# Optimization experiments

Hardware: AMD Instinct MI355X
Metric: run time of the kernel (lower is better)

## Reference

```python
import jax, jax.numpy as jnp
import numpy as np

BOX = 256          # box_size
N_CLASSES = 2      # n_classes
BATCH = 2
N_PTS = 262144


def setup_inputs() -> dict:
    key = jax.random.key(0)
    k1, k2 = jax.random.split(key)
    # points are normalized coordinates in [-0.5, 0.5)
    points = jax.random.uniform(k1, (BATCH, N_PTS, 3), dtype=jnp.float32,
                                minval=-0.5, maxval=0.499)
    values = jax.random.normal(k2, (BATCH, N_CLASSES, N_PTS), dtype=jnp.float32)
    return {"points": points, "values": values}


def reference(points, values):
    """Trilinear (CIC) scatter of per-point, per-class values into a 3D volume.

    points: [B, N, 3] in [-0.5, 0.5);  values: [B, C, N]
    returns vol: [B, C, box, box, box]
    """
    box = BOX
    V = box ** 3
    B, N, _ = points.shape
    C = values.shape[1]

    p = (points + 0.5) * box                 # [B, N, 3] voxel-space coords
    base = jnp.floor(p)
    r = p - base                              # fractional part, [B, N, 3]
    base = base.astype(jnp.int32)

    idx_list, w_list = [], []
    for dx in (0, 1):
        for dy in (0, 1):
            for dz in (0, 1):
                off_i = jnp.array([dx, dy, dz], dtype=jnp.int32)
                off_f = jnp.array([dx, dy, dz], dtype=r.dtype)
                c = base + off_i                                   # [B, N, 3]
                # per-axis weight: (1-d) + (2d-1)*r  == (1-r) if d=0 else r
                w = jnp.prod(1.0 - off_f + (2.0 * off_f - 1.0) * r, axis=-1)  # [B, N]
                x_, y_, z_ = c[..., 0], c[..., 1], c[..., 2]
                valid = ((x_ >= 0) & (x_ < box) & (y_ >= 0) & (y_ < box)
                         & (z_ >= 0) & (z_ < box))
                # out-of-range corners are redirected to index 0 with weight 0
                idx = ((z_ * box + y_) * box + x_) * valid.astype(jnp.int32)
                idx_list.append(idx)
                w_list.append(w * valid.astype(w.dtype))

    idx8 = jnp.concatenate(idx_list, axis=1)   # [B, 8N]
    w8 = jnp.concatenate(w_list, axis=1)       # [B, 8N]
    vals8 = jnp.tile(values, (1, 1, 8))        # [B, C, 8N]
    src = w8[:, None, :] * vals8               # [B, C, 8N]

    def scatter_one(idx_b, src_b):
        # idx_b: [8N], src_b: [C, 8N] -> [C, V]
        return jnp.zeros((C, V), src_b.dtype).at[:, idx_b].add(src_b)

    vol = jax.vmap(scatter_one)(idx8, src)     # [B, C, V]
    return vol.reshape(B, C, box, box, box)
```

## Files before the change

### kernel.cpp

```cpp
#include <hip/hip_runtime.h>

#define BOX   256
#define NCLS  2
#define BATCH 2
#define NPTS  262144
#define VOL   (BOX * BOX * BOX)
#define NBINS (BATCH * BOX * BOX)
#define CAP   32
#define CAPSH 5
#define RY    16
#define NT    (BOX / RY)
#define NREG  (BATCH * BOX * NT)
#define NBMETA 34

__global__ __launch_bounds__(256) void k_place(const float* __restrict__ pts,
                                               const float* __restrict__ vals,
                                               unsigned* __restrict__ cursor,
                                               float4* __restrict__ rec,
                                               float4* __restrict__ ovf4,
                                               unsigned* __restrict__ ovfbin,
                                               unsigned* __restrict__ ovfcnt)
{
    const int tid = blockIdx.x * 256 + threadIdx.x;
    const int b = tid >> 18;
    const int n = tid & (NPTS - 1);

    const float* pp = pts + ((size_t)b * NPTS + n) * 3;
    const float px = (pp[0] + 0.5f) * (float)BOX;
    const float py = (pp[1] + 0.5f) * (float)BOX;
    const float pz = (pp[2] + 0.5f) * (float)BOX;

    const float fy = floorf(py), fz = floorf(pz);
    const int by = (int)fy, bz = (int)fz;
    const float ry = py - fy, rz = pz - fz;

    const unsigned qy = (unsigned)(ry * 65536.0f);
    const unsigned qz = (unsigned)(rz * 65536.0f);
    const unsigned packed = (qz << 16) | (qy & 0xffffu);

    const float v0 = vals[((size_t)b * NCLS + 0) * NPTS + n];
    const float v1 = vals[((size_t)b * NCLS + 1) * NPTS + n];
    const float4 r = make_float4(px, __uint_as_float(packed), v0, v1);

    const unsigned bin = ((unsigned)b << 16) | ((unsigned)bz << 8) | (unsigned)by;
    const unsigned slot = atomicAdd(&cursor[bin], 1u);
    if (slot < CAP) {
        rec[((size_t)bin << CAPSH) + slot] = r;
    } else {
        const unsigned o = atomicAdd(ovfcnt, 1u);
        ovf4[o] = r;
        ovfbin[o] = bin;
    }
}

__global__ __launch_bounds__(512) void k_region(const float4* __restrict__ rec,
                                                const unsigned* __restrict__ cursor,
                                                const float4* __restrict__ ovf4,
                                                const unsigned* __restrict__ ovfbin,
                                                const unsigned* __restrict__ ovfcnt,
                                                float* __restrict__ out)
{
    __shared__ float acc[NCLS * RY * BOX];
    __shared__ unsigned s_bin[NBMETA];
    __shared__ unsigned s_len[NBMETA];
    __shared__ unsigned s_pfx[NBMETA + 1];

    const int tid = threadIdx.x;
    const int bid = blockIdx.x;
    const int b = bid >> 12;
    const int P = (bid >> 4) & 255;
    const int T = bid & 15;

    {
        float4* a4 = (float4*)acc;
        #pragma unroll
        for (int i = 0; i < 4; ++i)
            a4[i * 512 + tid] = make_float4(0.f, 0.f, 0.f, 0.f);
    }

    if (tid < NBMETA) {
        const int j = tid;
        const int zsrc = P - 1 + (j >= 17 ? 1 : 0);
        const int y0 = RY * T - 1 + (j >= 17 ? j - 17 : j);
        unsigned bin = 0, len = 0;
        if (zsrc >= 0 && y0 >= 0 && y0 < BOX) {
            bin = ((unsigned)b << 16) | ((unsigned)zsrc << 8) | (unsigned)y0;
            len = cursor[bin];
            if (len > CAP) len = CAP;
        }
        s_bin[j] = bin;
        s_len[j] = len;
    }
    __syncthreads();

    if (tid < 64) {
        const unsigned own = (tid < NBMETA) ? s_len[tid] : 0u;
        unsigned v = own;
        #pragma unroll
        for (int off = 1; off < 64; off <<= 1) {
            const unsigned t = __shfl_up(v, off, 64);
            if (tid >= off) v += t;
        }
        if (tid < NBMETA) s_pfx[tid] = v - own;
        if (tid == NBMETA - 1) s_pfx[NBMETA] = v;
    }
    __syncthreads();

    const int R = (int)s_pfx[NBMETA];
    for (int r = tid; r < R; r += 512) {
        int lo = 0, hi = NBMETA - 1;
        while (lo < hi) {
            const int mid = (lo + hi + 1) >> 1;
            if ((int)s_pfx[mid] <= r) lo = mid; else hi = mid - 1;
        }
        const size_t idx = ((size_t)s_bin[lo] << CAPSH) + (unsigned)(r - (int)s_pfx[lo]);
        const float4 q = rec[idx];

        const unsigned pk = __float_as_uint(q.y);
        const float ry = (float)(pk & 0xffffu) * (1.0f / 65536.0f);
        const float rz = (float)(pk >> 16) * (1.0f / 65536.0f);
        const float fx = floorf(q.x);
        const float rx = q.x - fx;
        const int ix = (int)fx;

        const float wz = (lo >= 17) ? (1.0f - rz) : rz;
        const int yy0 = (lo >= 17 ? lo - 17 : lo) - 1;

        #pragma unroll
        for (int dy = 0; dy < 2; ++dy) {
            const int yy = yy0 + dy;
            if ((unsigned)yy < RY) {
                const float wzy = wz * (dy ? ry : 1.0f - ry);
                #pragma unroll
                for (int dx = 0; dx < 2; ++dx) {
                    const int x = ix + dx;
                    if (x < BOX) {
                        const float w = wzy * (dx ? rx : 1.0f - rx);
                        const int li = yy * BOX + x;
                        atomicAdd(&acc[li], w * q.z);
                        atomicAdd(&acc[RY * BOX + li], w * q.w);
                    }
                }
            }
        }
    }

    const int oc = (int)*ovfcnt;
    for (int r = tid; r < oc; r += 512) {
        const unsigned bin = ovfbin[r];
        if ((int)(bin >> 16) != b) continue;
        const int bz = (int)((bin >> 8) & 255u);
        if (bz != P && bz != P - 1) continue;
        const int by = (int)(bin & 255u);
        const int yy0 = by - RY * T;
        if (yy0 < -1 || yy0 > RY - 1) continue;

        const float4 q = ovf4[r];
        const unsigned pk = __float_as_uint(q.y);
        const float ry = (float)(pk & 0xffffu) * (1.0f / 65536.0f);
        const float rz = (float)(pk >> 16) * (1.0f / 65536.0f);
        const float fx = floorf(q.x);
        const float rx = q.x - fx;
        const int ix = (int)fx;
        const float wz = (bz == P) ? (1.0f - rz) : rz;

        for (int dy = 0; dy < 2; ++dy) {
            const int yy = yy0 + dy;
            if ((unsigned)yy < RY) {
                const float wzy = wz * (dy ? ry : 1.0f - ry);
                for (int dx = 0; dx < 2; ++dx) {
                    const int x = ix + dx;
                    if (x < BOX) {
                        const float w = wzy * (dx ? rx : 1.0f - rx);
                        const int li = yy * BOX + x;
                        atomicAdd(&acc[li], w * q.z);
                        atomicAdd(&acc[RY * BOX + li], w * q.w);
                    }
                }
            }
        }
    }
    __syncthreads();

    #pragma unroll
    for (int c = 0; c < NCLS; ++c) {
        const size_t o4base = (size_t)((b * NCLS + c) * BOX + P) * (BOX * BOX / 4)
                              + (size_t)T * (RY * BOX / 4);
        float4* o4 = (float4*)out;
        const float4* a4 = (const float4*)(acc + c * RY * BOX);
        #pragma unroll
        for (int i = 0; i < 2; ++i)
            o4[o4base + i * 512 + tid] = a4[i * 512 + tid];
    }
}

__global__ __launch_bounds__(256) void cic_scatter_kernel(
    const float* __restrict__ points, const float* __restrict__ values,
    float* __restrict__ out)
{
    const int tid = blockIdx.x * blockDim.x + threadIdx.x;
    if (tid >= BATCH * NPTS) return;
    const int b = tid >> 18, n = tid & (NPTS - 1);
    const float* pp = points + ((size_t)b * NPTS + n) * 3;
    const float px = (pp[0] + 0.5f) * BOX, py = (pp[1] + 0.5f) * BOX, pz = (pp[2] + 0.5f) * BOX;
    const float fx = floorf(px), fy = floorf(py), fz = floorf(pz);
    const float rx = px - fx, ry = py - fy, rz = pz - fz;
    const int ix = (int)fx, iy = (int)fy, iz = (int)fz;
    const float v0 = values[((size_t)b * NCLS + 0) * NPTS + n];
    const float v1 = values[((size_t)b * NCLS + 1) * NPTS + n];
    const float wx[2] = {1.f - rx, rx}, wy[2] = {1.f - ry, ry}, wz[2] = {1.f - rz, rz};
    float* out0 = out + ((size_t)b * NCLS + 0) * (size_t)VOL;
    float* out1 = out + ((size_t)b * NCLS + 1) * (size_t)VOL;
    for (int dz = 0; dz < 2; ++dz) {
        const int z = iz + dz; if (z >= BOX) continue;
        for (int dy = 0; dy < 2; ++dy) {
            const int y = iy + dy; if (y >= BOX) continue;
            const float wzy = wz[dz] * wy[dy];
            const int rowbase = (z * BOX + y) * BOX;
            for (int dx = 0; dx < 2; ++dx) {
                const int x = ix + dx; if (x >= BOX) continue;
                atomicAdd(out0 + rowbase + x, wzy * wx[dx] * v0);
                atomicAdd(out1 + rowbase + x, wzy * wx[dx] * v1);
            }
        }
    }
}

extern "C" void kernel_launch(void* const* d_in, const int* in_sizes, int n_in,
                              void* d_out, int out_size, void* d_ws, size_t ws_size,
                              hipStream_t stream) {
    const float* points = (const float*)d_in[0];
    const float* values = (const float*)d_in[1];
    float* out = (float*)d_out;

    const size_t CUR_OFF  = 0;
    const size_t OVFC_OFF = (size_t)NBINS * 4;
    const size_t REC_OFF  = OVFC_OFF + 256;
    const size_t OVF4_OFF = REC_OFF + (size_t)NBINS * CAP * 16;
    const size_t OVFB_OFF = OVF4_OFF + (size_t)BATCH * NPTS * 16;
    const size_t WS_NEED  = OVFB_OFF + (size_t)BATCH * NPTS * 4;

    if (ws_size < WS_NEED) {
        hipMemsetAsync(out, 0, (size_t)out_size * sizeof(float), stream);
        cic_scatter_kernel<<<(BATCH * NPTS) / 256, 256, 0, stream>>>(points, values, out);
        return;
    }

    char* ws = (char*)d_ws;
    unsigned* cursor = (unsigned*)(ws + CUR_OFF);
    unsigned* ovfcnt = (unsigned*)(ws + OVFC_OFF);
    float4*   rec    = (float4*)(ws + REC_OFF);
    float4*   ovf4   = (float4*)(ws + OVF4_OFF);
    unsigned* ovfbin = (unsigned*)(ws + OVFB_OFF);

    hipMemsetAsync(ws, 0, OVFC_OFF + 256, stream);

    k_place<<<(BATCH * NPTS) / 256, 256, 0, stream>>>(points, values, cursor,
                                                      rec, ovf4, ovfbin, ovfcnt);
    k_region<<<NREG, 512, 0, stream>>>(rec, cursor, ovf4, ovfbin, ovfcnt, out);
}
```

Baseline: 112.8 us.

## Replace per-bin atomic binning with two-level block-local counting sort

Points are binned with a two-pass counting sort instead of one global atomic per point into fixed 32-slot bins. The first pass does a block-local histogram over coarse (batch, z-pair) groups, then coalesced staged writes. The second pass sorts each group by fine (z parity, y) bin and emits bin start and count tables. The region kernel then reads two contiguous ranges with no prefix-sum or binary search. Records now pack integer x plus quantized fractions. The cost is an extra kernel and another full pass over the records, and x precision drops to 15 bits.

```diff
diff --git a/kernel.cpp b/kernel.cpp
--- a/kernel.cpp
+++ b/kernel.cpp
@@ -1,71 +1,190 @@
 #include <hip/hip_runtime.h>
 
-#define BOX   256
-#define NCLS  2
-#define BATCH 2
-#define NPTS  262144
-#define VOL   (BOX * BOX * BOX)
-#define NBINS (BATCH * BOX * BOX)
-#define CAP   32
-#define CAPSH 5
-#define RY    16
-#define NT    (BOX / RY)
-#define NREG  (BATCH * BOX * NT)
-#define NBMETA 34
-
-__global__ __launch_bounds__(256) void k_place(const float* __restrict__ pts,
-                                               const float* __restrict__ vals,
-                                               unsigned* __restrict__ cursor,
-                                               float4* __restrict__ rec,
-                                               float4* __restrict__ ovf4,
-                                               unsigned* __restrict__ ovfbin,
-                                               unsigned* __restrict__ ovfcnt)
-{
-    const int tid = blockIdx.x * 256 + threadIdx.x;
-    const int b = tid >> 18;
-    const int n = tid & (NPTS - 1);
-
-    const float* pp = pts + ((size_t)b * NPTS + n) * 3;
-    const float px = (pp[0] + 0.5f) * (float)BOX;
-    const float py = (pp[1] + 0.5f) * (float)BOX;
-    const float pz = (pp[2] + 0.5f) * (float)BOX;
-
-    const float fy = floorf(py), fz = floorf(pz);
-    const int by = (int)fy, bz = (int)fz;
-    const float ry = py - fy, rz = pz - fz;
-
-    const unsigned qy = (unsigned)(ry * 65536.0f);
-    const unsigned qz = (unsigned)(rz * 65536.0f);
-    const unsigned packed = (qz << 16) | (qy & 0xffffu);
-
-    const float v0 = vals[((size_t)b * NCLS + 0) * NPTS + n];
-    const float v1 = vals[((size_t)b * NCLS + 1) * NPTS + n];
-    const float4 r = make_float4(px, __uint_as_float(packed), v0, v1);
-
-    const unsigned bin = ((unsigned)b << 16) | ((unsigned)bz << 8) | (unsigned)by;
-    const unsigned slot = atomicAdd(&cursor[bin], 1u);
-    if (slot < CAP) {
-        rec[((size_t)bin << CAPSH) + slot] = r;
-    } else {
-        const unsigned o = atomicAdd(ovfcnt, 1u);
-        ovf4[o] = r;
-        ovfbin[o] = bin;
-    }
-}
-
-__global__ __launch_bounds__(512) void k_region(const float4* __restrict__ rec,
-                                                const unsigned* __restrict__ cursor,
-                                                const float4* __restrict__ ovf4,
+#define BOX    256
+#define NCLS   2
+#define BATCH  2
+#define NPTS   262144
+#define VOL    (BOX * BOX * BOX)
+#define NPTOT  (BATCH * NPTS)
+#define NGRP   256
+#define GCAP   3584
+#define NFINE  512
+#define NBINS  (NGRP * NFINE)
+#define L1PTS  2048
+#define L1BLK  (NPTOT / L1PTS)
+#define RY     16
+#define NREG   (BATCH * BOX * (BOX / RY))
+
+__global__ __launch_bounds__(512) void k_zero(unsigned* __restrict__ p)
+{
+    p[threadIdx.x] = 0u;
+}
+
+__global__ __launch_bounds__(256) void k_l1(const float* __restrict__ pts,
+                                            const float* __restrict__ vals,
+                                            unsigned* __restrict__ gcur,
+                                            uint4* __restrict__ rec1,
+                                            uint4* __restrict__ ovf4,
+                                            unsigned* __restrict__ ovfbin,
+                                            unsigned* __restrict__ ovfcnt)
+{
+    __shared__ unsigned hist[256];
+    __shared__ unsigned excl[256];
+    __shared__ unsigned cur[256];
+    __shared__ unsigned gbase[256];
+    __shared__ uint4 stag[L1PTS];
+
+    const int t = threadIdx.x;
+    hist[t] = 0;
+    __syncthreads();
+
+    uint4 rec[8];
+    unsigned bkt[8];
+    const int base = blockIdx.x * L1PTS;
+    #pragma unroll
+    for (int k = 0; k < 8; ++k) {
+        const int gp = base + k * 256 + t;
+        const int b = gp >> 18;
+        const int n = gp & (NPTS - 1);
+        const float* pp = pts + (size_t)gp * 3;
+        const float px = (pp[0] + 0.5f) * 256.0f;
+        const float py = (pp[1] + 0.5f) * 256.0f;
+        const float pz = (pp[2] + 0.5f) * 256.0f;
+        const float fx = floorf(px), fy = floorf(py), fz = floorf(pz);
+        const int ix = (int)fx, by = (int)fy, bz = (int)fz;
+        const unsigned qx = (unsigned)((px - fx) * 32768.0f);
+        const unsigned qy = (unsigned)((py - fy) * 65536.0f);
+        const unsigned qz = (unsigned)((pz - fz) * 65536.0f);
+        const float v0 = vals[(size_t)(b * 2) * NPTS + n];
+        const float v1 = vals[(size_t)(b * 2 + 1) * NPTS + n];
+        rec[k].x = (unsigned)ix | (qx << 8) | ((unsigned)(bz & 1) << 23)
+                 | ((unsigned)by << 24);
+        rec[k].y = (qy & 0xffffu) | (qz << 16);
+        rec[k].z = __float_as_uint(v0);
+        rec[k].w = __float_as_uint(v1);
+        bkt[k] = ((unsigned)b << 7) | ((unsigned)bz >> 1);
+        atomicAdd(&hist[bkt[k]], 1u);
+    }
+    __syncthreads();
+
+    const unsigned own = hist[t];
+    for (int off = 1; off < 256; off <<= 1) {
+        unsigned v = 0;
+        if (t >= off) v = hist[t - off];
+        __syncthreads();
+        hist[t] += v;
+        __syncthreads();
+    }
+    const unsigned incl = hist[t];
+    const unsigned ex = incl - own;
+    excl[t] = ex;
+    cur[t] = ex;
+    if (own) gbase[t] = atomicAdd(&gcur[t], own);
+    __syncthreads();
+
+    #pragma unroll
+    for (int k = 0; k < 8; ++k) {
+        const unsigned s = atomicAdd(&cur[bkt[k]], 1u);
+        stag[s] = rec[k];
+    }
+    __syncthreads();
+
+    for (int s = t; s < L1PTS; s += 256) {
+        int lo = 0, hi = 255;
+        while (lo < hi) {
+            const int mid = (lo + hi) >> 1;
+            if (cur[mid] > (unsigned)s) hi = mid; else lo = mid + 1;
+        }
+        const unsigned rel = s - excl[lo];
+        const unsigned gaddr = gbase[lo] + rel;
+        const uint4 r = stag[s];
+        if (gaddr < GCAP) {
+            rec1[(size_t)lo * GCAP + gaddr] = r;
+        } else {
+            const unsigned o = atomicAdd(ovfcnt, 1u);
+            const unsigned zl = (r.x >> 23) & 1u;
+            const unsigned by = r.x >> 24;
+            ovf4[o] = r;
+            ovfbin[o] = ((unsigned)lo << 9) | (zl << 8) | by;
+        }
+    }
+}
+
+__global__ __launch_bounds__(512) void k_l2(const uint4* __restrict__ rec1,
+                                            const unsigned* __restrict__ gcur,
+                                            uint4* __restrict__ rec2,
+                                            unsigned* __restrict__ binStart,
+                                            unsigned* __restrict__ binCnt)
+{
+    __shared__ unsigned hist[NFINE];
+    __shared__ unsigned excl[NFINE];
+    __shared__ unsigned cur[NFINE];
+    __shared__ uint4 stag[GCAP];
+
+    const int t = threadIdx.x;
+    const int g = blockIdx.x;
+    hist[t] = 0;
+    __syncthreads();
+
+    unsigned cnt = gcur[g];
+    if (cnt > GCAP) cnt = GCAP;
+
+    uint4 rec[7];
+    unsigned fk[7];
+    #pragma unroll
+    for (int k = 0; k < 7; ++k) {
+        const int s = t + k * 512;
+        if (s < (int)cnt) {
+            const uint4 r = rec1[(size_t)g * GCAP + s];
+            const unsigned key = (((r.x >> 23) & 1u) << 8) | (r.x >> 24);
+            rec[k] = r; fk[k] = key;
+            atomicAdd(&hist[key], 1u);
+        }
+    }
+    __syncthreads();
+
+    const unsigned own = hist[t];
+    for (int off = 1; off < 512; off <<= 1) {
+        unsigned v = 0;
+        if (t >= off) v = hist[t - off];
+        __syncthreads();
+        hist[t] += v;
+        __syncthreads();
+    }
+    const unsigned incl = hist[t];
+    const unsigned ex = incl - own;
+    excl[t] = ex;
+    cur[t] = ex;
+    binStart[(g << 9) + t] = (unsigned)(g * GCAP) + ex;
+    binCnt[(g << 9) + t] = own;
+    __syncthreads();
+
+    #pragma unroll
+    for (int k = 0; k < 7; ++k) {
+        const int s = t + k * 512;
+        if (s < (int)cnt) {
+            const unsigned sl = atomicAdd(&cur[fk[k]], 1u);
+            stag[sl] = rec[k];
+        }
+    }
+    __syncthreads();
+
+    for (int s = t; s < (int)cnt; s += 512)
+        rec2[(size_t)g * GCAP + s] = stag[s];
+}
+
+__global__ __launch_bounds__(512) void k_region(const uint4* __restrict__ rec2,
+                                                const unsigned* __restrict__ binStart,
+                                                const unsigned* __restrict__ binCnt,
+                                                const uint4* __restrict__ ovf4,
                                                 const unsigned* __restrict__ ovfbin,
                                                 const unsigned* __restrict__ ovfcnt,
                                                 float* __restrict__ out)
 {
     __shared__ float acc[NCLS * RY * BOX];
-    __shared__ unsigned s_bin[NBMETA];
-    __shared__ unsigned s_len[NBMETA];
-    __shared__ unsigned s_pfx[NBMETA + 1];
-
-    const int tid = threadIdx.x;
+    __shared__ unsigned meta[4];
+
+    const int t = threadIdx.x;
     const int bid = blockIdx.x;
     const int b = bid >> 12;
     const int P = (bid >> 4) & 255;
@@ -75,56 +194,39 @@
         float4* a4 = (float4*)acc;
         #pragma unroll
         for (int i = 0; i < 4; ++i)
-            a4[i * 512 + tid] = make_float4(0.f, 0.f, 0.f, 0.f);
-    }
-
-    if (tid < NBMETA) {
-        const int j = tid;
-        const int zsrc = P - 1 + (j >= 17 ? 1 : 0);
-        const int y0 = RY * T - 1 + (j >= 17 ? j - 17 : j);
-        unsigned bin = 0, len = 0;
-        if (zsrc >= 0 && y0 >= 0 && y0 < BOX) {
-            bin = ((unsigned)b << 16) | ((unsigned)zsrc << 8) | (unsigned)y0;
-            len = cursor[bin];
-            if (len > CAP) len = CAP;
-        }
-        s_bin[j] = bin;
-        s_len[j] = len;
-    }
-    __syncthreads();
-
-    if (tid < 64) {
-        const unsigned own = (tid < NBMETA) ? s_len[tid] : 0u;
-        unsigned v = own;
-        #pragma unroll
-        for (int off = 1; off < 64; off <<= 1) {
-            const unsigned t = __shfl_up(v, off, 64);
-            if (tid >= off) v += t;
-        }
-        if (tid < NBMETA) s_pfx[tid] = v - own;
-        if (tid == NBMETA - 1) s_pfx[NBMETA] = v;
-    }
-    __syncthreads();
-
-    const int R = (int)s_pfx[NBMETA];
-    for (int r = tid; r < R; r += 512) {
-        int lo = 0, hi = NBMETA - 1;
-        while (lo < hi) {
-            const int mid = (lo + hi + 1) >> 1;
-            if ((int)s_pfx[mid] <= r) lo = mid; else hi = mid - 1;
-        }
-        const size_t idx = ((size_t)s_bin[lo] << CAPSH) + (unsigned)(r - (int)s_pfx[lo]);
-        const float4 q = rec[idx];
-
-        const unsigned pk = __float_as_uint(q.y);
-        const float ry = (float)(pk & 0xffffu) * (1.0f / 65536.0f);
-        const float rz = (float)(pk >> 16) * (1.0f / 65536.0f);
-        const float fx = floorf(q.x);
-        const float rx = q.x - fx;
-        const int ix = (int)fx;
-
-        const float wz = (lo >= 17) ? (1.0f - rz) : rz;
-        const int yy0 = (lo >= 17 ? lo - 17 : lo) - 1;
+            a4[i * 512 + t] = make_float4(0.f, 0.f, 0.f, 0.f);
+    }
+    if (t < 2) {
+        const int zsrc = P - 1 + t;
+        unsigned s = 0, e = 0;
+        if (zsrc >= 0) {
+            int ylo = 16 * T - 1; if (ylo < 0) ylo = 0;
+            const int yhi = 16 * T + 15;
+            const unsigned fb_lo = ((unsigned)b << 16) | ((unsigned)zsrc << 8) | (unsigned)ylo;
+            const unsigned fb_hi = ((unsigned)b << 16) | ((unsigned)zsrc << 8) | (unsigned)yhi;
+            s = binStart[fb_lo];
+            e = binStart[fb_hi] + binCnt[fb_hi];
+        }
+        meta[2 * t] = s; meta[2 * t + 1] = e;
+    }
+    __syncthreads();
+
+    const unsigned s1 = meta[0], e1 = meta[1], s2 = meta[2], e2 = meta[3];
+    const int n1 = (int)(e1 - s1), n2 = (int)(e2 - s2), n = n1 + n2;
+
+    for (int r = t; r < n; r += 512) {
+        const int inP = (r >= n1);
+        const unsigned idx = inP ? (s2 + (unsigned)(r - n1)) : (s1 + (unsigned)r);
+        const uint4 q = rec2[idx];
+        const int ix = (int)(q.x & 255u);
+        const float rx = (float)((q.x >> 8) & 0x7fffu) * (1.0f / 32768.0f);
+        const int by = (int)(q.x >> 24);
+        const float ry = (float)(q.y & 0xffffu) * (1.0f / 65536.0f);
+        const float rz = (float)(q.y >> 16) * (1.0f / 65536.0f);
+        const float v0 = __uint_as_float(q.z);
+        const float v1 = __uint_as_float(q.w);
+        const float wz = inP ? (1.0f - rz) : rz;
+        const int yy0 = by - 16 * T;
 
         #pragma unroll
         for (int dy = 0; dy < 2; ++dy) {
@@ -137,8 +239,8 @@
                     if (x < BOX) {
                         const float w = wzy * (dx ? rx : 1.0f - rx);
                         const int li = yy * BOX + x;
-                        atomicAdd(&acc[li], w * q.z);
-                        atomicAdd(&acc[RY * BOX + li], w * q.w);
+                        atomicAdd(&acc[li], w * v0);
+                        atomicAdd(&acc[RY * BOX + li], w * v1);
                     }
                 }
             }
@@ -146,24 +248,20 @@
     }
 
     const int oc = (int)*ovfcnt;
-    for (int r = tid; r < oc; r += 512) {
-        const unsigned bin = ovfbin[r];
-        if ((int)(bin >> 16) != b) continue;
-        const int bz = (int)((bin >> 8) & 255u);
+    for (int r = t; r < oc; r += 512) {
+        const unsigned fb = ovfbin[r];
+        if ((int)(fb >> 16) != b) continue;
+        const int bz = (int)((fb >> 8) & 255u);
         if (bz != P && bz != P - 1) continue;
-        const int by = (int)(bin & 255u);
-        const int yy0 = by - RY * T;
+        const int by = (int)(fb & 255u);
+        const int yy0 = by - 16 * T;
         if (yy0 < -1 || yy0 > RY - 1) continue;
-
-        const float4 q = ovf4[r];
-        const unsigned pk = __float_as_uint(q.y);
-        const float ry = (float)(pk & 0xffffu) * (1.0f / 65536.0f);
-        const float rz = (float)(pk >> 16) * (1.0f / 65536.0f);
-        const float fx = floorf(q.x);
-        const float rx = q.x - fx;
-        const int ix = (int)fx;
+        const uint4 q = ovf4[r];
+        const int ix = (int)(q.x & 255u);
+        const float rx = (float)((q.x >> 8) & 0x7fffu) * (1.0f / 32768.0f);
+        const float ry = (float)(q.y & 0xffffu) * (1.0f / 65536.0f);
+        const float rz = (float)(q.y >> 16) * (1.0f / 65536.0f);
         const float wz = (bz == P) ? (1.0f - rz) : rz;
-
         for (int dy = 0; dy < 2; ++dy) {
             const int yy = yy0 + dy;
             if ((unsigned)yy < RY) {
@@ -173,8 +271,8 @@
                     if (x < BOX) {
                         const float w = wzy * (dx ? rx : 1.0f - rx);
                         const int li = yy * BOX + x;
-                        atomicAdd(&acc[li], w * q.z);
-                        atomicAdd(&acc[RY * BOX + li], w * q.w);
+                        atomicAdd(&acc[li], w * __uint_as_float(q.z));
+                        atomicAdd(&acc[RY * BOX + li], w * __uint_as_float(q.w));
                     }
                 }
             }
@@ -190,7 +288,7 @@
         const float4* a4 = (const float4*)(acc + c * RY * BOX);
         #pragma unroll
         for (int i = 0; i < 2; ++i)
-            o4[o4base + i * 512 + tid] = a4[i * 512 + tid];
+            o4[o4base + i * 512 + t] = a4[i * 512 + t];
     }
 }
 
@@ -199,18 +297,18 @@
     float* __restrict__ out)
 {
     const int tid = blockIdx.x * blockDim.x + threadIdx.x;
-    if (tid >= BATCH * NPTS) return;
+    if (tid >= NPTOT) return;
     const int b = tid >> 18, n = tid & (NPTS - 1);
-    const float* pp = points + ((size_t)b * NPTS + n) * 3;
+    const float* pp = points + (size_t)tid * 3;
     const float px = (pp[0] + 0.5f) * BOX, py = (pp[1] + 0.5f) * BOX, pz = (pp[2] + 0.5f) * BOX;
     const float fx = floorf(px), fy = floorf(py), fz = floorf(pz);
     const float rx = px - fx, ry = py - fy, rz = pz - fz;
     const int ix = (int)fx, iy = (int)fy, iz = (int)fz;
-    const float v0 = values[((size_t)b * NCLS + 0) * NPTS + n];
-    const float v1 = values[((size_t)b * NCLS + 1) * NPTS + n];
+    const float v0 = values[(size_t)(b * 2) * NPTS + n];
+    const float v1 = values[(size_t)(b * 2 + 1) * NPTS + n];
     const float wx[2] = {1.f - rx, rx}, wy[2] = {1.f - ry, ry}, wz[2] = {1.f - rz, rz};
-    float* out0 = out + ((size_t)b * NCLS + 0) * (size_t)VOL;
-    float* out1 = out + ((size_t)b * NCLS + 1) * (size_t)VOL;
+    float* out0 = out + (size_t)(b * 2) * VOL;
+    float* out1 = out + (size_t)(b * 2 + 1) * VOL;
     for (int dz = 0; dz < 2; ++dz) {
         const int z = iz + dz; if (z >= BOX) continue;
         for (int dy = 0; dy < 2; ++dy) {
@@ -233,29 +331,34 @@
     const float* values = (const float*)d_in[1];
     float* out = (float*)d_out;
 
-    const size_t CUR_OFF  = 0;
-    const size_t OVFC_OFF = (size_t)NBINS * 4;
-    const size_t REC_OFF  = OVFC_OFF + 256;
-    const size_t OVF4_OFF = REC_OFF + (size_t)NBINS * CAP * 16;
-    const size_t OVFB_OFF = OVF4_OFF + (size_t)BATCH * NPTS * 16;
-    const size_t WS_NEED  = OVFB_OFF + (size_t)BATCH * NPTS * 4;
+    const size_t GCUR_OFF = 0;
+    const size_t OVFC_OFF = 1024;
+    const size_t REC1_OFF = 4096;
+    const size_t REC2_OFF = REC1_OFF + (size_t)NGRP * GCAP * 16;
+    const size_t BST_OFF  = REC2_OFF + (size_t)NGRP * GCAP * 16;
+    const size_t BCT_OFF  = BST_OFF + (size_t)NBINS * 4;
+    const size_t OVF4_OFF = BCT_OFF + (size_t)NBINS * 4;
+    const size_t OVFB_OFF = OVF4_OFF + (size_t)NPTOT * 16;
+    const size_t WS_NEED  = OVFB_OFF + (size_t)NPTOT * 4;
 
     if (ws_size < WS_NEED) {
         hipMemsetAsync(out, 0, (size_t)out_size * sizeof(float), stream);
-        cic_scatter_kernel<<<(BATCH * NPTS) / 256, 256, 0, stream>>>(points, values, out);
+        cic_scatter_kernel<<<NPTOT / 256, 256, 0, stream>>>(points, values, out);
         return;
     }
 
     char* ws = (char*)d_ws;
-    unsigned* cursor = (unsigned*)(ws + CUR_OFF);
-    unsigned* ovfcnt = (unsigned*)(ws + OVFC_OFF);
-    float4*   rec    = (float4*)(ws + REC_OFF);
-    float4*   ovf4   = (float4*)(ws + OVF4_OFF);
-    unsigned* ovfbin = (unsigned*)(ws + OVFB_OFF);
-
-    hipMemsetAsync(ws, 0, OVFC_OFF + 256, stream);
-
-    k_place<<<(BATCH * NPTS) / 256, 256, 0, stream>>>(points, values, cursor,
-                                                      rec, ovf4, ovfbin, ovfcnt);
-    k_region<<<NREG, 512, 0, stream>>>(rec, cursor, ovf4, ovfbin, ovfcnt, out);
-}
+    unsigned* gcur     = (unsigned*)(ws + GCUR_OFF);
+    unsigned* ovfcnt   = (unsigned*)(ws + OVFC_OFF);
+    uint4*    rec1     = (uint4*)(ws + REC1_OFF);
+    uint4*    rec2     = (uint4*)(ws + REC2_OFF);
+    unsigned* binStart = (unsigned*)(ws + BST_OFF);
+    unsigned* binCnt   = (unsigned*)(ws + BCT_OFF);
+    uint4*    ovf4     = (uint4*)(ws + OVF4_OFF);
+    unsigned* ovfbin   = (unsigned*)(ws + OVFB_OFF);
+
+    k_zero<<<1, 512, 0, stream>>>((unsigned*)ws);
+    k_l1<<<L1BLK, 256, 0, stream>>>(points, values, gcur, rec1, ovf4, ovfbin, ovfcnt);
+    k_l2<<<NGRP, 512, 0, stream>>>(rec1, gcur, rec2, binStart, binCnt);
+    k_region<<<NREG, 512, 0, stream>>>(rec2, binStart, binCnt, ovf4, ovfbin, ovfcnt, out);
+}
```

After: 118.3 us. 4.9% more time.
